# Performance work log

Hardware: AMD Instinct MI355X
Metric: run time of the kernel (lower is better)

## Reference

```python
import jax, jax.numpy as jnp
import numpy as np

N_NODES = 50000
N_EDGES = 600000
D = 128


def setup_inputs() -> dict:
    key = jax.random.key(0)
    ks = jax.random.split(key, 12)
    s = 1.0 / np.sqrt(D)
    inp = {
        "node_features": jax.random.normal(ks[0], (N_NODES, D), dtype=jnp.float32),
        "from_idx": jax.random.randint(ks[1], (N_EDGES,), 0, N_NODES),
        "to_idx": jax.random.randint(ks[2], (N_EDGES,), 0, N_NODES),
        # message net: Linear(2D->256), Linear(256->128), ReLU after each
        "msg_W0": jax.random.uniform(ks[3], (2 * D, 256), jnp.float32, -s, s),
        "msg_b0": jax.random.uniform(ks[4], (256,), jnp.float32, -s, s),
        "msg_W1": jax.random.uniform(ks[5], (256, D), jnp.float32, -s, s),
        "msg_b1": jax.random.uniform(ks[6], (D,), jnp.float32, -s, s),
        # node update MLP: Linear(2D->256), Linear(256->D), ReLU after each, residual
        "upd_W0": jax.random.uniform(ks[7], (2 * D, 256), jnp.float32, -s, s),
        "upd_b0": jax.random.uniform(ks[8], (256,), jnp.float32, -s, s),
        "upd_W1": jax.random.uniform(ks[9], (256, D), jnp.float32, -s, s),
        "upd_b1": jax.random.uniform(ks[10], (D,), jnp.float32, -s, s),
    }
    return inp


def reference(node_features, from_idx, to_idx,
              msg_W0, msg_b0, msg_W1, msg_b1,
              upd_W0, upd_b0, upd_W1, upd_b1):
    # --- message computation: gather endpoint features, concat, LRL MLP (relu after every layer) ---
    from_feat = node_features[from_idx]            # [E, D]
    to_feat = node_features[to_idx]                # [E, D]
    m = jnp.concatenate([from_feat, to_feat], axis=-1)  # [E, 2D]
    m = jax.nn.relu(m @ msg_W0 + msg_b0)
    m = jax.nn.relu(m @ msg_W1 + msg_b1)           # [E, D]
    # --- aggregate: unsorted segment sum onto destination nodes ---
    agg = jax.ops.segment_sum(m, to_idx, num_segments=N_NODES)  # [N, D]
    # --- node update (residual): MLP on [agg, node_features] then add ---
    h = jnp.concatenate([agg, node_features], axis=-1)  # [N, 2D]
    h = jax.nn.relu(h @ upd_W0 + upd_b0)
    h = jax.nn.relu(h @ upd_W1 + upd_b1)           # [N, D]
    return node_features + h
```

## Files before the change

kernel.cpp:

```cpp
#include <hip/hip_runtime.h>

#define NN 50000
#define NE 600000
#define DD 128
#define XS 264
#define NB 49

typedef unsigned short u16;
typedef u16   u16x8  __attribute__((ext_vector_type(8)));
typedef u16   u16x4  __attribute__((ext_vector_type(4)));
typedef __bf16 bf16x8 __attribute__((ext_vector_type(8)));
typedef float f32x4  __attribute__((ext_vector_type(4)));

__device__ __forceinline__ u16 f2bf(float f) {
    unsigned u = __builtin_bit_cast(unsigned, f);
    u += 0x7FFFu + ((u >> 16) & 1u);
    return (u16)(u >> 16);
}

__device__ __forceinline__ void loadB(bf16x8 (&d)[8], const u16* __restrict__ pw, int nt, int lane) {
    #pragma unroll
    for (int kt = 0; kt < 8; ++kt)
        d[kt] = __builtin_bit_cast(bf16x8, *(const u16x8*)(pw + (nt * 8 + kt) * 512 + lane * 8));
}

__device__ __forceinline__ void pack_one(const float* __restrict__ W, u16* __restrict__ out,
                                         int K, int N, int tid) {
    int frag = tid >> 9, lane = (tid >> 3) & 63, j = tid & 7;
    int KT = K >> 5;
    int nt = frag / KT, kt = frag - nt * KT;
    int row = kt * 32 + ((lane >> 4) << 3) + j;
    int col = nt * 16 + (lane & 15);
    out[tid] = f2bf(W[row * N + col]);
}

__global__ void k_prep(const float* __restrict__ nf, u16* __restrict__ nf16,
                       const int* __restrict__ to_idx, int* __restrict__ cnt,
                       const float* __restrict__ mW0, u16* __restrict__ pmW0,
                       const float* __restrict__ mW1, u16* __restrict__ pmW1,
                       const float* __restrict__ uW0, u16* __restrict__ puW0,
                       const float* __restrict__ uW1, u16* __restrict__ puW1)
{
    const int b = blockIdx.x;
    const int tid = threadIdx.x;
    if (b < 6250) {
        int id = b * 256 + tid;
        float4 v = ((const float4*)nf)[id];
        u16x4 o; o[0] = f2bf(v.x); o[1] = f2bf(v.y); o[2] = f2bf(v.z); o[3] = f2bf(v.w);
        ((u16x4*)nf16)[id] = o;
    } else if (b < 6250 + 2344) {
        int e = (b - 6250) * 256 + tid;
        if (e < NE) atomicAdd(&cnt[to_idx[e]], 1);
    } else {
        int g = (b - 8594) * 256 + tid;
        if (g < 65536)       pack_one(mW0, pmW0, 256, 256, g);
        else if (g < 98304)  pack_one(mW1, pmW1, 256, 128, g - 65536);
        else if (g < 163840) pack_one(uW0, puW0, 256, 256, g - 98304);
        else                 pack_one(uW1, puW1, 256, 128, g - 163840);
    }
}

__global__ void k_scanA(const int* __restrict__ cnt, int* __restrict__ part, int* __restrict__ bsum) {
    __shared__ int s[1024];
    int tid = threadIdx.x;
    int g = blockIdx.x * 1024 + tid;
    int v = (g < NN) ? cnt[g] : 0;
    s[tid] = v;
    __syncthreads();
    for (int ofs = 1; ofs < 1024; ofs <<= 1) {
        int t = (tid >= ofs) ? s[tid - ofs] : 0;
        __syncthreads();
        s[tid] += t;
        __syncthreads();
    }
    if (g < NN) part[g] = s[tid] - v;
    if (tid == 1023) bsum[blockIdx.x] = s[1023];
}

__global__ void k_scanC(const int* __restrict__ part, const int* __restrict__ bsum, int* __restrict__ cursor) {
    int g = blockIdx.x * 256 + threadIdx.x;
    if (g < NN) {
        int blk = g >> 10;
        int off = 0;
        for (int j = 0; j < blk; ++j) off += bsum[j];
        cursor[g] = part[g] + off;
    }
}

__global__ void k_reorder(const int* __restrict__ from_idx, const int* __restrict__ to_idx,
                          int* __restrict__ cursor, int2* __restrict__ est) {
    int e = blockIdx.x * 256 + threadIdx.x;
    if (e < NE) {
        int d = to_idx[e];
        int p = atomicAdd(&cursor[d], 1);
        est[p] = make_int2(from_idx[e], d);
    }
}

__global__ __launch_bounds__(128, 2) void k_edges(
    const u16* __restrict__ nf16, const int2* __restrict__ est,
    const u16* __restrict__ pW0, const float* __restrict__ b0,
    const u16* __restrict__ pW1, const float* __restrict__ b1,
    float* __restrict__ agg)
{
    __shared__ u16 sX[64 * XS];
    __shared__ int sDest[64];
    const int tid = threadIdx.x;
    const int lane = tid & 63;
    const int wave = tid >> 6;
    const int base = wave * 32;
    const int l15  = lane & 15;
    const int quad = lane >> 4;
    const int e0 = blockIdx.x * 64;

    if (tid < 64) sDest[tid] = est[e0 + tid].y;

    float bias0[16], bias1[8];
    #pragma unroll
    for (int nt = 0; nt < 16; ++nt) bias0[nt] = b0[nt * 16 + l15];
    #pragma unroll
    for (int nt = 0; nt < 8; ++nt)  bias1[nt] = b1[nt * 16 + l15];

    #pragma unroll
    for (int i = 0; i < 16; ++i) {
        int c = i * 128 + tid;
        int r = c >> 5, j = c & 31;
        int2 ft = est[e0 + r];
        int node = (j < 16) ? ft.x : ft.y;
        *(u16x8*)(&sX[r * XS + j * 8]) = *(const u16x8*)(nf16 + node * DD + (j & 15) * 8);
    }
    __syncthreads();

    const int arow0 = (base + l15) * XS + quad * 8;

    bf16x8 a[2][8];
    #pragma unroll
    for (int mt = 0; mt < 2; ++mt)
        #pragma unroll
        for (int kt = 0; kt < 8; ++kt)
            a[mt][kt] = __builtin_bit_cast(bf16x8, *(const u16x8*)(&sX[arow0 + mt * 16 * XS + kt * 32]));

    bf16x8 bA[8], bB[8];
    loadB(bA, pW0, 0, lane);
    #pragma unroll
    for (int np = 0; np < 8; ++np) {
        const int ntA = 2 * np, ntB = 2 * np + 1;
        loadB(bB, pW0, ntB, lane);
        __builtin_amdgcn_sched_barrier(0);
        f32x4 c0 = {0.f, 0.f, 0.f, 0.f}, c1 = {0.f, 0.f, 0.f, 0.f};
        #pragma unroll
        for (int kt = 0; kt < 8; ++kt) {
            c0 = __builtin_amdgcn_mfma_f32_16x16x32_bf16(a[0][kt], bA[kt], c0, 0, 0, 0);
            c1 = __builtin_amdgcn_mfma_f32_16x16x32_bf16(a[1][kt], bA[kt], c1, 0, 0, 0);
        }
        #pragma unroll
        for (int i = 0; i < 4; ++i) {
            sX[(base +      quad * 4 + i) * XS + ntA * 16 + l15] = f2bf(fmaxf(c0[i] + bias0[ntA], 0.f));
            sX[(base + 16 + quad * 4 + i) * XS + ntA * 16 + l15] = f2bf(fmaxf(c1[i] + bias0[ntA], 0.f));
        }
        if (np < 7) {
            loadB(bA, pW0, ntA + 2, lane);
            __builtin_amdgcn_sched_barrier(0);
        }
        f32x4 d0 = {0.f, 0.f, 0.f, 0.f}, d1 = {0.f, 0.f, 0.f, 0.f};
        #pragma unroll
        for (int kt = 0; kt < 8; ++kt) {
            d0 = __builtin_amdgcn_mfma_f32_16x16x32_bf16(a[0][kt], bB[kt], d0, 0, 0, 0);
            d1 = __builtin_amdgcn_mfma_f32_16x16x32_bf16(a[1][kt], bB[kt], d1, 0, 0, 0);
        }
        #pragma unroll
        for (int i = 0; i < 4; ++i) {
            sX[(base +      quad * 4 + i) * XS + ntB * 16 + l15] = f2bf(fmaxf(d0[i] + bias0[ntB], 0.f));
            sX[(base + 16 + quad * 4 + i) * XS + ntB * 16 + l15] = f2bf(fmaxf(d1[i] + bias0[ntB], 0.f));
        }
    }

    #pragma unroll
    for (int mt = 0; mt < 2; ++mt)
        #pragma unroll
        for (int kt = 0; kt < 8; ++kt)
            a[mt][kt] = __builtin_bit_cast(bf16x8, *(const u16x8*)(&sX[arow0 + mt * 16 * XS + kt * 32]));

    __syncthreads();

    float* sM = (float*)sX;
    loadB(bA, pW1, 0, lane);
    #pragma unroll
    for (int np = 0; np < 4; ++np) {
        const int ntA = 2 * np, ntB = 2 * np + 1;
        loadB(bB, pW1, ntB, lane);
        __builtin_amdgcn_sched_barrier(0);
        f32x4 c0 = {0.f, 0.f, 0.f, 0.f}, c1 = {0.f, 0.f, 0.f, 0.f};
        #pragma unroll
        for (int kt = 0; kt < 8; ++kt) {
            c0 = __builtin_amdgcn_mfma_f32_16x16x32_bf16(a[0][kt], bA[kt], c0, 0, 0, 0);
            c1 = __builtin_amdgcn_mfma_f32_16x16x32_bf16(a[1][kt], bA[kt], c1, 0, 0, 0);
        }
        #pragma unroll
        for (int i = 0; i < 4; ++i) {
            sM[(base +      quad * 4 + i) * 132 + ntA * 16 + l15] = fmaxf(c0[i] + bias1[ntA], 0.f);
            sM[(base + 16 + quad * 4 + i) * 132 + ntA * 16 + l15] = fmaxf(c1[i] + bias1[ntA], 0.f);
        }
        if (np < 3) {
            loadB(bA, pW1, ntA + 2, lane);
            __builtin_amdgcn_sched_barrier(0);
        }
        f32x4 d0 = {0.f, 0.f, 0.f, 0.f}, d1 = {0.f, 0.f, 0.f, 0.f};
        #pragma unroll
        for (int kt = 0; kt < 8; ++kt) {
            d0 = __builtin_amdgcn_mfma_f32_16x16x32_bf16(a[0][kt], bB[kt], d0, 0, 0, 0);
            d1 = __builtin_amdgcn_mfma_f32_16x16x32_bf16(a[1][kt], bB[kt], d1, 0, 0, 0);
        }
        #pragma unroll
        for (int i = 0; i < 4; ++i) {
            sM[(base +      quad * 4 + i) * 132 + ntB * 16 + l15] = fmaxf(d0[i] + bias1[ntB], 0.f);
            sM[(base + 16 + quad * 4 + i) * 132 + ntB * 16 + l15] = fmaxf(d1[i] + bias1[ntB], 0.f);
        }
    }
    __syncthreads();

    const int head_d = sDest[0];
    const int tail_d = sDest[63];
    const bool head_sh = (e0 > 0) && (est[e0 - 1].y == head_d);
    const bool tail_sh = (e0 + 64 < NE) && (est[e0 + 64].y == tail_d);

    int dprev = head_d;
    float acc = sM[tid];
    for (int r = 1; r < 64; ++r) {
        int d = sDest[r];
        float v = sM[r * 132 + tid];
        if (d == dprev) acc += v;
        else {
            if ((dprev == head_d && head_sh) || (dprev == tail_d && tail_sh))
                unsafeAtomicAdd(&agg[(size_t)dprev * DD + tid], acc);
            else
                agg[(size_t)dprev * DD + tid] = acc;
            acc = v; dprev = d;
        }
    }
    if ((dprev == head_d && head_sh) || (dprev == tail_d && tail_sh))
        unsafeAtomicAdd(&agg[(size_t)dprev * DD + tid], acc);
    else
        agg[(size_t)dprev * DD + tid] = acc;
}

__global__ __launch_bounds__(64, 2) void k_update(
    const float* __restrict__ agg, const u16* __restrict__ nf16,
    const float* __restrict__ nf32, const u16* __restrict__ pW0,
    const float* __restrict__ b0, const u16* __restrict__ pW1,
    const float* __restrict__ b1, float* __restrict__ out)
{
    __shared__ u16 sX[32 * XS];
    const int lane = threadIdx.x;
    const int l15  = lane & 15;
    const int quad = lane >> 4;
    const int n0 = blockIdx.x * 32;

    float bias0[16], bias1[8];
    #pragma unroll
    for (int nt = 0; nt < 16; ++nt) bias0[nt] = b0[nt * 16 + l15];
    #pragma unroll
    for (int nt = 0; nt < 8; ++nt)  bias1[nt] = b1[nt * 16 + l15];

    #pragma unroll
    for (int i = 0; i < 16; ++i) {
        int c = i * 64 + lane;
        int r = c >> 5, j = c & 31;
        int n = n0 + r;
        u16x4 o;
        if (n < NN) {
            float4 v = *(const float4*)(agg + (size_t)n * DD + j * 4);
            o[0] = f2bf(v.x); o[1] = f2bf(v.y); o[2] = f2bf(v.z); o[3] = f2bf(v.w);
        } else { o[0] = 0; o[1] = 0; o[2] = 0; o[3] = 0; }
        *(u16x4*)(&sX[r * XS + j * 4]) = o;
    }
    #pragma unroll
    for (int i = 0; i < 8; ++i) {
        int c = i * 64 + lane;
        int r = c >> 4, j = c & 15;
        int n = n0 + r;
        u16x8 v = {0, 0, 0, 0, 0, 0, 0, 0};
        if (n < NN) v = *(const u16x8*)(nf16 + (size_t)n * DD + j * 8);
        *(u16x8*)(&sX[r * XS + 128 + j * 8]) = v;
    }

    const int arow0 = l15 * XS + quad * 8;

    bf16x8 a[2][8];
    #pragma unroll
    for (int mt = 0; mt < 2; ++mt)
        #pragma unroll
        for (int kt = 0; kt < 8; ++kt)
            a[mt][kt] = __builtin_bit_cast(bf16x8, *(const u16x8*)(&sX[arow0 + mt * 16 * XS + kt * 32]));

    bf16x8 bA[8], bB[8];
    loadB(bA, pW0, 0, lane);
    #pragma unroll
    for (int np = 0; np < 8; ++np) {
        const int ntA = 2 * np, ntB = 2 * np + 1;
        loadB(bB, pW0, ntB, lane);
        __builtin_amdgcn_sched_barrier(0);
        f32x4 c0 = {0.f, 0.f, 0.f, 0.f}, c1 = {0.f, 0.f, 0.f, 0.f};
        #pragma unroll
        for (int kt = 0; kt < 8; ++kt) {
            c0 = __builtin_amdgcn_mfma_f32_16x16x32_bf16(a[0][kt], bA[kt], c0, 0, 0, 0);
            c1 = __builtin_amdgcn_mfma_f32_16x16x32_bf16(a[1][kt], bA[kt], c1, 0, 0, 0);
        }
        #pragma unroll
        for (int i = 0; i < 4; ++i) {
            sX[(     quad * 4 + i) * XS + ntA * 16 + l15] = f2bf(fmaxf(c0[i] + bias0[ntA], 0.f));
            sX[(16 + quad * 4 + i) * XS + ntA * 16 + l15] = f2bf(fmaxf(c1[i] + bias0[ntA], 0.f));
        }
        if (np < 7) {
            loadB(bA, pW0, ntA + 2, lane);
            __builtin_amdgcn_sched_barrier(0);
        }
        f32x4 d0 = {0.f, 0.f, 0.f, 0.f}, d1 = {0.f, 0.f, 0.f, 0.f};
        #pragma unroll
        for (int kt = 0; kt < 8; ++kt) {
            d0 = __builtin_amdgcn_mfma_f32_16x16x32_bf16(a[0][kt], bB[kt], d0, 0, 0, 0);
            d1 = __builtin_amdgcn_mfma_f32_16x16x32_bf16(a[1][kt], bB[kt], d1, 0, 0, 0);
        }
        #pragma unroll
        for (int i = 0; i < 4; ++i) {
            sX[(     quad * 4 + i) * XS + ntB * 16 + l15] = f2bf(fmaxf(d0[i] + bias0[ntB], 0.f));
            sX[(16 + quad * 4 + i) * XS + ntB * 16 + l15] = f2bf(fmaxf(d1[i] + bias0[ntB], 0.f));
        }
    }

    #pragma unroll
    for (int mt = 0; mt < 2; ++mt)
        #pragma unroll
        for (int kt = 0; kt < 8; ++kt)
            a[mt][kt] = __builtin_bit_cast(bf16x8, *(const u16x8*)(&sX[arow0 + mt * 16 * XS + kt * 32]));

    loadB(bA, pW1, 0, lane);
    #pragma unroll
    for (int np = 0; np < 4; ++np) {
        const int ntA = 2 * np, ntB = 2 * np + 1;
        loadB(bB, pW1, ntB, lane);
        __builtin_amdgcn_sched_barrier(0);
        f32x4 c0 = {0.f, 0.f, 0.f, 0.f}, c1 = {0.f, 0.f, 0.f, 0.f};
        #pragma unroll
        for (int kt = 0; kt < 8; ++kt) {
            c0 = __builtin_amdgcn_mfma_f32_16x16x32_bf16(a[0][kt], bA[kt], c0, 0, 0, 0);
            c1 = __builtin_amdgcn_mfma_f32_16x16x32_bf16(a[1][kt], bA[kt], c1, 0, 0, 0);
        }
        {
            int col = ntA * 16 + l15;
            #pragma unroll
            for (int i = 0; i < 4; ++i) {
                int na = n0 +      quad * 4 + i;
                int nb = n0 + 16 + quad * 4 + i;
                if (na < NN) out[(size_t)na * DD + col] = nf32[(size_t)na * DD + col] + fmaxf(c0[i] + bias1[ntA], 0.f);
                if (nb < NN) out[(size_t)nb * DD + col] = nf32[(size_t)nb * DD + col] + fmaxf(c1[i] + bias1[ntA], 0.f);
            }
        }
        if (np < 3) {
            loadB(bA, pW1, ntA + 2, lane);
            __builtin_amdgcn_sched_barrier(0);
        }
        f32x4 d0 = {0.f, 0.f, 0.f, 0.f}, d1 = {0.f, 0.f, 0.f, 0.f};
        #pragma unroll
        for (int kt = 0; kt < 8; ++kt) {
            d0 = __builtin_amdgcn_mfma_f32_16x16x32_bf16(a[0][kt], bB[kt], d0, 0, 0, 0);
            d1 = __builtin_amdgcn_mfma_f32_16x16x32_bf16(a[1][kt], bB[kt], d1, 0, 0, 0);
        }
        {
            int col = ntB * 16 + l15;
            #pragma unroll
            for (int i = 0; i < 4; ++i) {
                int na = n0 +      quad * 4 + i;
                int nb = n0 + 16 + quad * 4 + i;
                if (na < NN) out[(size_t)na * DD + col] = nf32[(size_t)na * DD + col] + fmaxf(d0[i] + bias1[ntB], 0.f);
                if (nb < NN) out[(size_t)nb * DD + col] = nf32[(size_t)nb * DD + col] + fmaxf(d1[i] + bias1[ntB], 0.f);
            }
        }
    }
}

extern "C" void kernel_launch(void* const* d_in, const int* in_sizes, int n_in,
                              void* d_out, int out_size, void* d_ws, size_t ws_size,
                              hipStream_t stream)
{
    const float* nf  = (const float*)d_in[0];
    const int* fidx  = (const int*)d_in[1];
    const int* tidx  = (const int*)d_in[2];
    const float* mW0 = (const float*)d_in[3];
    const float* mb0 = (const float*)d_in[4];
    const float* mW1 = (const float*)d_in[5];
    const float* mb1 = (const float*)d_in[6];
    const float* uW0 = (const float*)d_in[7];
    const float* ub0 = (const float*)d_in[8];
    const float* uW1 = (const float*)d_in[9];
    const float* ub1 = (const float*)d_in[10];
    float* out = (float*)d_out;

    char* ws = (char*)d_ws;
    u16*   nf16 = (u16*)ws;   ws += (size_t)NN * DD * 2;
    float* agg  = (float*)ws; ws += (size_t)NN * DD * 4;
    u16*   pmW0 = (u16*)ws;   ws += 256 * 256 * 2;
    u16*   pmW1 = (u16*)ws;   ws += 256 * 128 * 2;
    u16*   puW0 = (u16*)ws;   ws += 256 * 256 * 2;
    u16*   puW1 = (u16*)ws;   ws += 256 * 128 * 2;
    int*   cnt    = (int*)ws; ws += (size_t)NN * 4;
    int*   cursor = (int*)ws; ws += (size_t)NN * 4;
    int*   part   = (int*)ws; ws += (size_t)NN * 4;
    int*   bsum   = (int*)ws; ws += 64 * 4;
    int2*  est    = (int2*)ws; ws += (size_t)NE * 8;

    hipMemsetAsync(agg, 0, (size_t)NN * DD * 4, stream);
    hipMemsetAsync(cnt, 0, (size_t)NN * 4, stream);
    k_prep<<<9362, 256, 0, stream>>>(nf, nf16, tidx, cnt, mW0, pmW0, mW1, pmW1, uW0, puW0, uW1, puW1);
    k_scanA<<<NB, 1024, 0, stream>>>(cnt, part, bsum);
    k_scanC<<<(NN + 255) / 256, 256, 0, stream>>>(part, bsum, cursor);
    k_reorder<<<(NE + 255) / 256, 256, 0, stream>>>(fidx, tidx, cursor, est);
    k_edges<<<NE / 64, 128, 0, stream>>>(nf16, est, pmW0, mb0, pmW1, mb1, agg);
    k_update<<<(NN + 31) / 32, 64, 0, stream>>>(agg, nf16, nf, puW0, ub0, puW1, ub1, out);
}
```

Before: 358.6 us.

## Precompute per-node to-feature half of first message layer

Splits the first message-layer GEMM: the to_idx half (nf16 @ W0[128:256]) is computed once per node in a new k_pre kernel and stored as fp32 in a 50000x256 buffer. The edge kernel then gathers only from-node features, seeds the MFMA accumulators with the precomputed per-destination rows, and runs half the K-dimension for layer 0. This removes half the layer-0 MFMA work per edge and half the feature gather, but adds an extra kernel and a 51 MB fp32 intermediate that must be written and then read back via random-access gathers.

```diff
diff --git a/kernel.cpp b/kernel.cpp
--- a/kernel.cpp
+++ b/kernel.cpp
@@ -21,6 +21,11 @@
 __device__ __forceinline__ void loadB(bf16x8 (&d)[8], const u16* __restrict__ pw, int nt, int lane) {
     #pragma unroll
     for (int kt = 0; kt < 8; ++kt)
+        d[kt] = __builtin_bit_cast(bf16x8, *(const u16x8*)(pw + (nt * 8 + kt) * 512 + lane * 8));
+}
+__device__ __forceinline__ void loadB4(bf16x8 (&d)[4], const u16* __restrict__ pw, int nt, int lane) {
+    #pragma unroll
+    for (int kt = 0; kt < 4; ++kt)
         d[kt] = __builtin_bit_cast(bf16x8, *(const u16x8*)(pw + (nt * 8 + kt) * 512 + lane * 8));
 }
 
@@ -60,6 +65,44 @@
     }
 }
 
+__global__ __launch_bounds__(128, 2) void k_pre(
+    const u16* __restrict__ nf16, const u16* __restrict__ pW0, float* __restrict__ yto)
+{
+    const int tid = threadIdx.x;
+    const int lane = tid & 63;
+    const int wave = tid >> 6;
+    const int base = wave * 32;
+    const int l15  = lane & 15;
+    const int quad = lane >> 4;
+    const int n0 = blockIdx.x * 64;
+
+    bf16x8 a[2][4];
+    #pragma unroll
+    for (int mt = 0; mt < 2; ++mt) {
+        int n = n0 + base + mt * 16 + l15; if (n >= NN) n = NN - 1;
+        #pragma unroll
+        for (int kt = 0; kt < 4; ++kt)
+            a[mt][kt] = __builtin_bit_cast(bf16x8, *(const u16x8*)(nf16 + (size_t)n * DD + kt * 32 + quad * 8));
+    }
+
+    for (int nt = 0; nt < 16; ++nt) {
+        f32x4 c0 = {0.f, 0.f, 0.f, 0.f}, c1 = {0.f, 0.f, 0.f, 0.f};
+        #pragma unroll
+        for (int kt = 0; kt < 4; ++kt) {
+            bf16x8 b = __builtin_bit_cast(bf16x8, *(const u16x8*)(pW0 + (nt * 8 + 4 + kt) * 512 + lane * 8));
+            c0 = __builtin_amdgcn_mfma_f32_16x16x32_bf16(a[0][kt], b, c0, 0, 0, 0);
+            c1 = __builtin_amdgcn_mfma_f32_16x16x32_bf16(a[1][kt], b, c1, 0, 0, 0);
+        }
+        #pragma unroll
+        for (int i = 0; i < 4; ++i) {
+            int na = n0 + base +      quad * 4 + i;
+            int nb = n0 + base + 16 + quad * 4 + i;
+            if (na < NN) yto[(size_t)na * 256 + nt * 16 + l15] = c0[i];
+            if (nb < NN) yto[(size_t)nb * 256 + nt * 16 + l15] = c1[i];
+        }
+    }
+}
+
 __global__ void k_scanA(const int* __restrict__ cnt, int* __restrict__ part, int* __restrict__ bsum) {
     __shared__ int s[1024];
     int tid = threadIdx.x;
@@ -101,7 +144,7 @@
     const u16* __restrict__ nf16, const int2* __restrict__ est,
     const u16* __restrict__ pW0, const float* __restrict__ b0,
     const u16* __restrict__ pW1, const float* __restrict__ b1,
-    float* __restrict__ agg)
+    const float* __restrict__ yto, float* __restrict__ agg)
 {
     __shared__ u16 sX[64 * XS];
     __shared__ int sDest[64];
@@ -122,79 +165,90 @@
     for (int nt = 0; nt < 8; ++nt)  bias1[nt] = b1[nt * 16 + l15];
 
     #pragma unroll
-    for (int i = 0; i < 16; ++i) {
+    for (int i = 0; i < 8; ++i) {
         int c = i * 128 + tid;
-        int r = c >> 5, j = c & 31;
-        int2 ft = est[e0 + r];
-        int node = (j < 16) ? ft.x : ft.y;
-        *(u16x8*)(&sX[r * XS + j * 8]) = *(const u16x8*)(nf16 + node * DD + (j & 15) * 8);
+        int r = c >> 4, j = c & 15;
+        *(u16x8*)(&sX[r * XS + j * 8]) = *(const u16x8*)(nf16 + (size_t)est[e0 + r].x * DD + j * 8);
     }
     __syncthreads();
 
     const int arow0 = (base + l15) * XS + quad * 8;
 
+    const float* yp0[4];
+    const float* yp1[4];
+    #pragma unroll
+    for (int i = 0; i < 4; ++i) {
+        yp0[i] = yto + (size_t)sDest[base +      quad * 4 + i] * 256 + l15;
+        yp1[i] = yto + (size_t)sDest[base + 16 + quad * 4 + i] * 256 + l15;
+    }
+
     bf16x8 a[2][8];
+    #pragma unroll
+    for (int mt = 0; mt < 2; ++mt)
+        #pragma unroll
+        for (int kt = 0; kt < 4; ++kt)
+            a[mt][kt] = __builtin_bit_cast(bf16x8, *(const u16x8*)(&sX[arow0 + mt * 16 * XS + kt * 32]));
+
+    bf16x8 bA[4], bB[4];
+    loadB4(bA, pW0, 0, lane);
+    #pragma unroll
+    for (int np = 0; np < 8; ++np) {
+        const int ntA = 2 * np, ntB = 2 * np + 1;
+        loadB4(bB, pW0, ntB, lane);
+        __builtin_amdgcn_sched_barrier(0);
+        f32x4 c0, c1;
+        #pragma unroll
+        for (int i = 0; i < 4; ++i) { c0[i] = yp0[i][ntA * 16]; c1[i] = yp1[i][ntA * 16]; }
+        #pragma unroll
+        for (int kt = 0; kt < 4; ++kt) {
+            c0 = __builtin_amdgcn_mfma_f32_16x16x32_bf16(a[0][kt], bA[kt], c0, 0, 0, 0);
+            c1 = __builtin_amdgcn_mfma_f32_16x16x32_bf16(a[1][kt], bA[kt], c1, 0, 0, 0);
+        }
+        #pragma unroll
+        for (int i = 0; i < 4; ++i) {
+            sX[(base +      quad * 4 + i) * XS + ntA * 16 + l15] = f2bf(fmaxf(c0[i] + bias0[ntA], 0.f));
+            sX[(base + 16 + quad * 4 + i) * XS + ntA * 16 + l15] = f2bf(fmaxf(c1[i] + bias0[ntA], 0.f));
+        }
+        if (np < 7) {
+            loadB4(bA, pW0, ntA + 2, lane);
+            __builtin_amdgcn_sched_barrier(0);
+        }
+        f32x4 d0, d1;
+        #pragma unroll
+        for (int i = 0; i < 4; ++i) { d0[i] = yp0[i][ntB * 16]; d1[i] = yp1[i][ntB * 16]; }
+        #pragma unroll
+        for (int kt = 0; kt < 4; ++kt) {
+            d0 = __builtin_amdgcn_mfma_f32_16x16x32_bf16(a[0][kt], bB[kt], d0, 0, 0, 0);
+            d1 = __builtin_amdgcn_mfma_f32_16x16x32_bf16(a[1][kt], bB[kt], d1, 0, 0, 0);
+        }
+        #pragma unroll
+        for (int i = 0; i < 4; ++i) {
+            sX[(base +      quad * 4 + i) * XS + ntB * 16 + l15] = f2bf(fmaxf(d0[i] + bias0[ntB], 0.f));
+            sX[(base + 16 + quad * 4 + i) * XS + ntB * 16 + l15] = f2bf(fmaxf(d1[i] + bias0[ntB], 0.f));
+        }
+    }
+
     #pragma unroll
     for (int mt = 0; mt < 2; ++mt)
         #pragma unroll
         for (int kt = 0; kt < 8; ++kt)
             a[mt][kt] = __builtin_bit_cast(bf16x8, *(const u16x8*)(&sX[arow0 + mt * 16 * XS + kt * 32]));
 
-    bf16x8 bA[8], bB[8];
-    loadB(bA, pW0, 0, lane);
-    #pragma unroll
-    for (int np = 0; np < 8; ++np) {
+    __syncthreads();
+
+    float* sM = (float*)sX;
+    bf16x8 eA[8], eB[8];
+    loadB(eA, pW1, 0, lane);
+    #pragma unroll
+    for (int np = 0; np < 4; ++np) {
         const int ntA = 2 * np, ntB = 2 * np + 1;
-        loadB(bB, pW0, ntB, lane);
+        loadB(eB, pW1, ntB, lane);
         __builtin_amdgcn_sched_barrier(0);
         f32x4 c0 = {0.f, 0.f, 0.f, 0.f}, c1 = {0.f, 0.f, 0.f, 0.f};
         #pragma unroll
         for (int kt = 0; kt < 8; ++kt) {
-            c0 = __builtin_amdgcn_mfma_f32_16x16x32_bf16(a[0][kt], bA[kt], c0, 0, 0, 0);
-            c1 = __builtin_amdgcn_mfma_f32_16x16x32_bf16(a[1][kt], bA[kt], c1, 0, 0, 0);
-        }
-        #pragma unroll
-        for (int i = 0; i < 4; ++i) {
-            sX[(base +      quad * 4 + i) * XS + ntA * 16 + l15] = f2bf(fmaxf(c0[i] + bias0[ntA], 0.f));
-            sX[(base + 16 + quad * 4 + i) * XS + ntA * 16 + l15] = f2bf(fmaxf(c1[i] + bias0[ntA], 0.f));
-        }
-        if (np < 7) {
-            loadB(bA, pW0, ntA + 2, lane);
-            __builtin_amdgcn_sched_barrier(0);
-        }
-        f32x4 d0 = {0.f, 0.f, 0.f, 0.f}, d1 = {0.f, 0.f, 0.f, 0.f};
-        #pragma unroll
-        for (int kt = 0; kt < 8; ++kt) {
-            d0 = __builtin_amdgcn_mfma_f32_16x16x32_bf16(a[0][kt], bB[kt], d0, 0, 0, 0);
-            d1 = __builtin_amdgcn_mfma_f32_16x16x32_bf16(a[1][kt], bB[kt], d1, 0, 0, 0);
-        }
-        #pragma unroll
-        for (int i = 0; i < 4; ++i) {
-            sX[(base +      quad * 4 + i) * XS + ntB * 16 + l15] = f2bf(fmaxf(d0[i] + bias0[ntB], 0.f));
-            sX[(base + 16 + quad * 4 + i) * XS + ntB * 16 + l15] = f2bf(fmaxf(d1[i] + bias0[ntB], 0.f));
-        }
-    }
-
-    #pragma unroll
-    for (int mt = 0; mt < 2; ++mt)
-        #pragma unroll
-        for (int kt = 0; kt < 8; ++kt)
-            a[mt][kt] = __builtin_bit_cast(bf16x8, *(const u16x8*)(&sX[arow0 + mt * 16 * XS + kt * 32]));
-
-    __syncthreads();
-
-    float* sM = (float*)sX;
-    loadB(bA, pW1, 0, lane);
-    #pragma unroll
-    for (int np = 0; np < 4; ++np) {
-        const int ntA = 2 * np, ntB = 2 * np + 1;
-        loadB(bB, pW1, ntB, lane);
-        __builtin_amdgcn_sched_barrier(0);
-        f32x4 c0 = {0.f, 0.f, 0.f, 0.f}, c1 = {0.f, 0.f, 0.f, 0.f};
-        #pragma unroll
-        for (int kt = 0; kt < 8; ++kt) {
-            c0 = __builtin_amdgcn_mfma_f32_16x16x32_bf16(a[0][kt], bA[kt], c0, 0, 0, 0);
-            c1 = __builtin_amdgcn_mfma_f32_16x16x32_bf16(a[1][kt], bA[kt], c1, 0, 0, 0);
+            c0 = __builtin_amdgcn_mfma_f32_16x16x32_bf16(a[0][kt], eA[kt], c0, 0, 0, 0);
+            c1 = __builtin_amdgcn_mfma_f32_16x16x32_bf16(a[1][kt], eA[kt], c1, 0, 0, 0);
         }
         #pragma unroll
         for (int i = 0; i < 4; ++i) {
@@ -202,14 +256,14 @@
             sM[(base + 16 + quad * 4 + i) * 132 + ntA * 16 + l15] = fmaxf(c1[i] + bias1[ntA], 0.f);
         }
         if (np < 3) {
-            loadB(bA, pW1, ntA + 2, lane);
+            loadB(eA, pW1, ntA + 2, lane);
             __builtin_amdgcn_sched_barrier(0);
         }
         f32x4 d0 = {0.f, 0.f, 0.f, 0.f}, d1 = {0.f, 0.f, 0.f, 0.f};
         #pragma unroll
         for (int kt = 0; kt < 8; ++kt) {
-            d0 = __builtin_amdgcn_mfma_f32_16x16x32_bf16(a[0][kt], bB[kt], d0, 0, 0, 0);
-            d1 = __builtin_amdgcn_mfma_f32_16x16x32_bf16(a[1][kt], bB[kt], d1, 0, 0, 0);
+            d0 = __builtin_amdgcn_mfma_f32_16x16x32_bf16(a[0][kt], eB[kt], d0, 0, 0, 0);
+            d1 = __builtin_amdgcn_mfma_f32_16x16x32_bf16(a[1][kt], eB[kt], d1, 0, 0, 0);
         }
         #pragma unroll
         for (int i = 0; i < 4; ++i) {
@@ -399,6 +453,7 @@
     char* ws = (char*)d_ws;
     u16*   nf16 = (u16*)ws;   ws += (size_t)NN * DD * 2;
     float* agg  = (float*)ws; ws += (size_t)NN * DD * 4;
+    float* yto  = (float*)ws; ws += (size_t)NN * 256 * 4;
     u16*   pmW0 = (u16*)ws;   ws += 256 * 256 * 2;
     u16*   pmW1 = (u16*)ws;   ws += 256 * 128 * 2;
     u16*   puW0 = (u16*)ws;   ws += 256 * 256 * 2;
@@ -412,9 +467,10 @@
     hipMemsetAsync(agg, 0, (size_t)NN * DD * 4, stream);
     hipMemsetAsync(cnt, 0, (size_t)NN * 4, stream);
     k_prep<<<9362, 256, 0, stream>>>(nf, nf16, tidx, cnt, mW0, pmW0, mW1, pmW1, uW0, puW0, uW1, puW1);
+    k_pre<<<(NN + 63) / 64, 128, 0, stream>>>(nf16, pmW0, yto);
     k_scanA<<<NB, 1024, 0, stream>>>(cnt, part, bsum);
     k_scanC<<<(NN + 255) / 256, 256, 0, stream>>>(part, bsum, cursor);
     k_reorder<<<(NE + 255) / 256, 256, 0, stream>>>(fidx, tidx, cursor, est);
-    k_edges<<<NE / 64, 128, 0, stream>>>(nf16, est, pmW0, mb0, pmW1, mb1, agg);
+    k_edges<<<NE / 64, 128, 0, stream>>>(nf16, est, pmW0, mb0, pmW1, mb1, yto, agg);
     k_update<<<(NN + 31) / 32, 64, 0, stream>>>(agg, nf16, nf, puW0, ub0, puW1, ub1, out);
 }
```

After: 381.0 us. +6.2%, slower.
